# Performance work log

Hardware: AMD Instinct MI355X
Metric: run time of the kernel (lower is better)

The kernel has to match this reference:

```python
import jax, jax.numpy as jnp
import numpy as np

HIDDEN = 640
NQ = 10      # query heads
NKV = 2      # kv heads
HD = HIDDEN // NQ   # 64
GROUPS = NQ // NKV  # 5
THETA = 500000.0
EPS = 1e-6


def rmsnorm(x, g):
    rms = jnp.sqrt(jnp.mean(x * x, axis=-1, keepdims=True) + EPS)
    return x / rms * g


def bitlinear(x, w, g):
    """RMSNorm + ternary weight / int8 activation fake-quant + GEMM + rescale."""
    x = rmsnorm(x, g)
    alpha = jnp.maximum(jnp.mean(jnp.abs(w)), 1e-10)
    w_q = jnp.clip(jnp.round(w / alpha), -1.0, 1.0)
    w_q = w + jax.lax.stop_gradient(w_q - w)            # STE
    gamma = jnp.maximum(jnp.max(jnp.abs(x), axis=-1, keepdims=True), 1e-10)
    x_q = jnp.clip(jnp.round(x * 127.0 / gamma), -128.0, 127.0)
    x_q = x + jax.lax.stop_gradient(x_q - x)            # STE
    return (x_q @ w_q.T) * (alpha * gamma / 127.0)


def rope_tables(L):
    # half-dim cos/sin tables [L, HD//2]; equivalent to the torch code's
    # repeat_interleave followed by [..., ::2] slicing.
    freqs = 1.0 / THETA ** (jnp.arange(0, HD, 2, dtype=jnp.float32) / HD)
    ang = jnp.arange(L, dtype=jnp.float32)[:, None] * freqs[None, :]
    return jnp.cos(ang), jnp.sin(ang)


def apply_rope(x, cos, sin):
    # x: [B,H,L,D]; cos/sin: [L,D/2] broadcast over B,H
    x1 = x[..., ::2]
    x2 = x[..., 1::2]
    o1 = x1 * cos - x2 * sin
    o2 = x2 * cos + x1 * sin
    return jnp.stack([o1, o2], axis=-1).reshape(x.shape)


def setup_inputs() -> dict:
    key = jax.random.key(0)
    ks = jax.random.split(key, 6)
    B, L = 32, 512
    x = jax.random.normal(ks[0], (B, L, HIDDEN), dtype=jnp.float32)
    s_h = 1.0 / np.sqrt(HIDDEN)
    q_w = jax.random.normal(ks[1], (NQ * HD, HIDDEN), dtype=jnp.float32) * s_h
    k_w = jax.random.normal(ks[2], (NKV * HD, HIDDEN), dtype=jnp.float32) * s_h
    v_w = jax.random.normal(ks[3], (NKV * HD, HIDDEN), dtype=jnp.float32) * s_h
    o_w = jax.random.normal(ks[4], (HIDDEN, NQ * HD), dtype=jnp.float32) * (1.0 / np.sqrt(NQ * HD))
    ones = jnp.ones((HIDDEN,), dtype=jnp.float32)
    return {
        "x": x,
        "norm_w": ones,
        "q_w": q_w, "q_g": ones,
        "k_w": k_w, "k_g": ones,
        "v_w": v_w, "v_g": ones,
        "o_w": o_w, "o_g": jnp.ones((NQ * HD,), dtype=jnp.float32),
    }


def reference(x, norm_w, q_w, q_g, k_w, k_g, v_w, v_g, o_w, o_g):
    B, L, _ = x.shape
    residual = x
    h = rmsnorm(x, norm_w)
    q = bitlinear(h, q_w, q_g).reshape(B, L, NQ, HD).transpose(0, 2, 1, 3)
    k = bitlinear(h, k_w, k_g).reshape(B, L, NKV, HD).transpose(0, 2, 1, 3)
    v = bitlinear(h, v_w, v_g).reshape(B, L, NKV, HD).transpose(0, 2, 1, 3)
    cos, sin = rope_tables(L)
    q = apply_rope(q, cos, sin)
    k = apply_rope(k, cos, sin)
    k = jnp.repeat(k, GROUPS, axis=1)   # [B,NQ,L,HD]
    v = jnp.repeat(v, GROUPS, axis=1)
    scale = 1.0 / np.sqrt(HD).astype(np.float32)
    attn = jnp.einsum("bhqd,bhkd->bhqk", q, k) * scale
    attn = jax.nn.softmax(attn, axis=-1)
    out = jnp.einsum("bhqk,bhkd->bhqd", attn, v)
    out = out.transpose(0, 2, 1, 3).reshape(B, L, NQ * HD)
    return bitlinear(out, o_w, o_g) + residual
```

## Files before the change

### kernel.cpp

```cpp
#include <hip/hip_runtime.h>
#include <math.h>
#include <stdint.h>

#define HIDDEN 640
#define NTOK   16384
#define LSEQ   512
#define BATCH  32
#define NQH    10
#define NKVH   2
#define HDIM   64
#define GROUPS 5

typedef int      int4v  __attribute__((ext_vector_type(4)));
typedef int      int16v __attribute__((ext_vector_type(16)));
typedef _Float16 f16x8  __attribute__((ext_vector_type(8)));
typedef _Float16 f16x2  __attribute__((ext_vector_type(2)));
typedef float    f32x4  __attribute__((ext_vector_type(4)));

__device__ __forceinline__ float wred_sum(float v){
  #pragma unroll
  for (int m=1;m<64;m<<=1) v += __shfl_xor(v,m);
  return v;
}
__device__ __forceinline__ float wred_max(float v){
  #pragma unroll
  for (int m=1;m<64;m<<=1) v = fmaxf(v,__shfl_xor(v,m));
  return v;
}
__device__ __forceinline__ f16x2 pkmax(f16x2 a, f16x2 b){
  f16x2 r;
  r.x = (a.x > b.x) ? a.x : b.x;
  r.y = (a.y > b.y) ? a.y : b.y;
  return r;
}
__device__ __forceinline__ f16x2 shflx(f16x2 v, int m){
  int t = __builtin_bit_cast(int, v);
  t = __shfl_xor(t, m);
  return __builtin_bit_cast(f16x2, t);
}

__global__ __launch_bounds__(256) void absum4_kernel(
    const float* __restrict__ w0, const float* __restrict__ w1,
    const float* __restrict__ w2, const float* __restrict__ w3,
    float* __restrict__ sums){
  const float* w; int n;
  switch(blockIdx.y){
    case 0:  w=w0; n=640*640; break;
    case 1:  w=w1; n=128*640; break;
    case 2:  w=w2; n=128*640; break;
    default: w=w3; n=640*640; break;
  }
  __shared__ float red[256];
  int tid = threadIdx.x;
  float s = 0.f;
  for (int i = blockIdx.x*256 + tid; i < n; i += gridDim.x*256) s += fabsf(w[i]);
  red[tid] = s; __syncthreads();
  for (int off=128; off>0; off>>=1){ if (tid<off) red[tid]+=red[tid+off]; __syncthreads(); }
  if (tid==0) atomicAdd(&sums[blockIdx.y], red[0]);
}

__global__ __launch_bounds__(256) void wquant4_kernel(
    const float* __restrict__ w0, const float* __restrict__ w1,
    const float* __restrict__ w2, const float* __restrict__ w3,
    int8_t* __restrict__ o0, int8_t* __restrict__ o1,
    int8_t* __restrict__ o2, int8_t* __restrict__ o3,
    const float* __restrict__ sums){
  const float* w; int8_t* o; int n;
  switch(blockIdx.y){
    case 0:  w=w0; o=o0; n=640*640; break;
    case 1:  w=w1; o=o1; n=128*640; break;
    case 2:  w=w2; o=o2; n=128*640; break;
    default: w=w3; o=o3; n=640*640; break;
  }
  float alpha = fmaxf(sums[blockIdx.y]/(float)n, 1e-10f);
  float inva  = 1.0f/alpha;
  int i = blockIdx.x*256 + threadIdx.x;
  if (i < n){
    float t = rintf(w[i]*inva);
    t = fminf(1.f, fmaxf(-1.f, t));
    int nr = i/640;
    int kc = i - nr*640;
    int flat = (((nr>>5)*20 + (kc>>5))<<10) + (((((kc>>4)&1)<<5) | (nr&31))<<4) + (kc&15);
    o[flat] = (int8_t)t;
  }
}

__global__ __launch_bounds__(256) void token_prep_kernel(
    const float* __restrict__ x, const float* __restrict__ nw,
    const float* __restrict__ qg, const float* __restrict__ kg, const float* __restrict__ vg,
    int8_t* __restrict__ xqq, int8_t* __restrict__ xqk, int8_t* __restrict__ xqv,
    float* __restrict__ gq, float* __restrict__ gk, float* __restrict__ gv){
  int lane = threadIdx.x & 63;
  int m = blockIdx.x*4 + (threadIdx.x>>6);
  const float* xr = x + (size_t)m*HIDDEN;
  float xv[10], h[10];
  float ss = 0.f;
  #pragma unroll
  for (int j=0;j<10;j++){ float t = xr[lane + 64*j]; xv[j]=t; ss += t*t; }
  float inv1 = 1.0f/sqrtf(wred_sum(ss)*(1.0f/HIDDEN) + 1e-6f);
  float ss2 = 0.f;
  #pragma unroll
  for (int j=0;j<10;j++){ float t = xv[j]*inv1*nw[lane+64*j]; h[j]=t; ss2 += t*t; }
  float inv2 = 1.0f/sqrtf(wred_sum(ss2)*(1.0f/HIDDEN) + 1e-6f);

  const float* gs[3] = {qg, kg, vg};
  int8_t* outs[3] = {xqq, xqk, xqv};
  float* gams[3] = {gq, gk, gv};
  #pragma unroll
  for (int s=0;s<3;s++){
    const float* g = gs[s];
    float t[10], amax = 0.f;
    #pragma unroll
    for (int j=0;j<10;j++){ float v = h[j]*inv2*g[lane+64*j]; t[j]=v; amax = fmaxf(amax, fabsf(v)); }
    float gamma = fmaxf(wred_max(amax), 1e-10f);
    float sc = 127.0f/gamma;
    int8_t* dst = outs[s] + (size_t)m*HIDDEN;
    #pragma unroll
    for (int j=0;j<10;j++){
      float v = rintf(t[j]*sc);
      v = fminf(127.f, fmaxf(-128.f, v));
      dst[lane+64*j] = (int8_t)v;
    }
    if (lane==0) gams[s][m] = gamma;
  }
}

__global__ __launch_bounds__(256) void o_prep_kernel(const _Float16* __restrict__ ao,
    const float* __restrict__ og, int8_t* __restrict__ xqo, float* __restrict__ go){
  int lane = threadIdx.x & 63;
  int m = blockIdx.x*4 + (threadIdx.x>>6);
  const _Float16* xr = ao + (size_t)m*HIDDEN;
  float xv[10];
  float ss = 0.f;
  #pragma unroll
  for (int j=0;j<10;j++){ float t = (float)xr[lane + 64*j]; xv[j]=t; ss += t*t; }
  float inv = 1.0f/sqrtf(wred_sum(ss)*(1.0f/HIDDEN) + 1e-6f);
  float t[10], amax = 0.f;
  #pragma unroll
  for (int j=0;j<10;j++){ float v = xv[j]*inv*og[lane+64*j]; t[j]=v; amax = fmaxf(amax, fabsf(v)); }
  float gamma = fmaxf(wred_max(amax), 1e-10f);
  float sc = 127.0f/gamma;
  int8_t* dst = xqo + (size_t)m*HIDDEN;
  #pragma unroll
  for (int j=0;j<10;j++){
    float v = rintf(t[j]*sc);
    v = fminf(127.f, fmaxf(-128.f, v));
    dst[lane+64*j] = (int8_t)v;
  }
  if (lane==0) go[m] = gamma;
}

__device__ __forceinline__ void gemm_core(
    const int8_t* __restrict__ xq, const int8_t* __restrict__ wqf,
    int m0, int n0, int lane, int16v& acc0, int16v& acc1){
  int half = lane >> 5, lan5 = lane & 31;
  const int8_t* arow = xq + (size_t)(m0 + lan5)*HIDDEN + half*16;
  const int8_t* b0 = wqf + (((size_t)(n0>>5)    *20)<<10) + (lane<<4);
  const int8_t* b1 = wqf + (((size_t)((n0>>5)+1)*20)<<10) + (lane<<4);
  #pragma unroll
  for (int kb=0; kb<20; kb++){
    int4v a  = *(const int4v*)(arow + kb*32);
    int4v v0 = *(const int4v*)(b0 + (kb<<10));
    int4v v1 = *(const int4v*)(b1 + (kb<<10));
    acc0 = __builtin_amdgcn_mfma_i32_32x32x32_i8(a, v0, acc0, 0, 0, 0);
    acc1 = __builtin_amdgcn_mfma_i32_32x32x32_i8(a, v1, acc1, 0, 0, 0);
  }
}

__global__ __launch_bounds__(256) void qkv_gemm_kernel(
    const int8_t* __restrict__ xq_q, const float* __restrict__ g_q, const int8_t* __restrict__ wq_q,
    const int8_t* __restrict__ xq_k, const float* __restrict__ g_k, const int8_t* __restrict__ wq_k,
    const int8_t* __restrict__ xq_v, const float* __restrict__ g_v, const int8_t* __restrict__ wq_v,
    const float* __restrict__ sums,
    _Float16* __restrict__ qbuf, _Float16* __restrict__ kbuf, _Float16* __restrict__ vbuf){
  __shared__ _Float16 Tr[4][64][40];
  int bx = blockIdx.x;
  const int8_t *xq, *wq; const float* gam; _Float16* outh;
  int n0, aidx, nheads, mode; float inv_nw, vscale;
  if (bx < 10){ xq=xq_q; wq=wq_q; gam=g_q; outh=qbuf; n0=bx*64;      aidx=0; inv_nw=1.0f/409600.f; nheads=NQH;  mode=1; vscale=0.125f; }
  else if (bx < 12){ xq=xq_k; wq=wq_k; gam=g_k; outh=kbuf; n0=(bx-10)*64; aidx=1; inv_nw=1.0f/81920.f; nheads=NKVH; mode=1; vscale=1.0f; }
  else { xq=xq_v; wq=wq_v; gam=g_v; outh=vbuf; n0=(bx-12)*64; aidx=2; inv_nw=1.0f/81920.f; nheads=NKVH; mode=2; vscale=1.0f; }

  int lane = threadIdx.x & 63;
  int w    = threadIdx.x >> 6;
  int m0   = blockIdx.y*128 + w*32;
  int half = lane >> 5, lan5 = lane & 31;

  int16v acc0 = {0}, acc1 = {0};
  gemm_core(xq, wq, m0, n0, lane, acc0, acc1);

  float alpha = fmaxf(sums[aidx]*inv_nw, 1e-10f);
  float fr0 = 0.f, fr1 = 0.f;
  if (mode == 1){
    int d0 = (lan5) & ~1;
    int d1 = (32 + lan5) & ~1;
    fr0 = __expf(-(float)d0*(1.0f/64.0f)*13.122363377404328f);
    fr1 = __expf(-(float)d1*(1.0f/64.0f)*13.122363377404328f);
  }

  #pragma unroll
  for (int reg=0; reg<16; reg++){
    int ml = (reg&3) + 8*(reg>>2) + 4*half;
    int m = m0 + ml;
    float sc = alpha*gam[m]*(1.0f/127.0f);
    float v0 = (float)acc0[reg]*sc;
    float v1 = (float)acc1[reg]*sc;
    if (mode == 1){
      int b = m >> 9, l = m & 511;
      int head = n0 >> 6;
      float p0 = __shfl_xor(v0, 1);
      float p1 = __shfl_xor(v1, 1);
      float sn0, cs0, sn1, cs1;
      __sincosf((float)l*fr0, &sn0, &cs0);
      __sincosf((float)l*fr1, &sn1, &cs1);
      if (lane & 1){ v0 = v0*cs0 + p0*sn0;  v1 = v1*cs1 + p1*sn1; }
      else         { v0 = v0*cs0 - p0*sn0;  v1 = v1*cs1 - p1*sn1; }
      _Float16* dst = outh + ((((size_t)b*nheads + head)*LSEQ + l)<<6);
      dst[lan5]      = (_Float16)(v0*vscale);
      dst[32 + lan5] = (_Float16)(v1*vscale);
    } else {
      Tr[w][lan5][ml]      = (_Float16)v0;
      Tr[w][32 + lan5][ml] = (_Float16)v1;
    }
  }
  if (mode == 2){
    int b = m0 >> 9, l0 = m0 & 511;
    int head = n0 >> 6;
    f16x8 r0 = *(const f16x8*)&Tr[w][lane][0];
    f16x8 r1 = *(const f16x8*)&Tr[w][lane][8];
    f16x8 r2 = *(const f16x8*)&Tr[w][lane][16];
    f16x8 r3 = *(const f16x8*)&Tr[w][lane][24];
    _Float16* dst = outh + (((size_t)b*nheads + head)*HDIM + lane)*LSEQ + l0;
    ((f16x8*)dst)[0] = r0;
    ((f16x8*)dst)[1] = r1;
    ((f16x8*)dst)[2] = r2;
    ((f16x8*)dst)[3] = r3;
  }
}

__global__ __launch_bounds__(256) void out_gemm_kernel(
    const int8_t* __restrict__ xq, const float* __restrict__ gam,
    const int8_t* __restrict__ wq, const float* __restrict__ sums,
    const float* __restrict__ resid, float* __restrict__ outf){
  int lane = threadIdx.x & 63;
  int w    = threadIdx.x >> 6;
  int m0   = blockIdx.y*128 + w*32;
  int n0   = blockIdx.x*64;
  int half = lane >> 5, lan5 = lane & 31;

  int16v acc0 = {0}, acc1 = {0};
  gemm_core(xq, wq, m0, n0, lane, acc0, acc1);

  float alpha = fmaxf(sums[3]*(1.0f/409600.f), 1e-10f);
  #pragma unroll
  for (int reg=0; reg<16; reg++){
    int m = m0 + (reg&3) + 8*(reg>>2) + 4*half;
    float sc = alpha*gam[m]*(1.0f/127.0f);
    size_t ofs = (size_t)m*HIDDEN;
    outf[ofs + n0 + lan5]      = (float)acc0[reg]*sc + resid[ofs + n0 + lan5];
    outf[ofs + n0 + 32 + lan5] = (float)acc1[reg]*sc + resid[ofs + n0 + 32 + lan5];
  }
}

__device__ __forceinline__ int kv_addr(int row, int chunk){
  return (row<<6) + (((chunk ^ (row&7)))<<3);
}

__device__ __forceinline__ void softmax_update(
    f32x4* S, float* m_i, float* l_i, f32x4* O,
    _Float16 (*PsRow)[72], int quad, int c){
  float mxr[4], psr[4];
  #pragma unroll
  for (int r=0;r<4;r++)
    mxr[r] = fmaxf(fmaxf(S[0][r],S[1][r]), fmaxf(S[2][r],S[3][r]));
  f16x2 a01 = {(_Float16)mxr[0], (_Float16)mxr[1]};
  f16x2 a23 = {(_Float16)mxr[2], (_Float16)mxr[3]};
  #pragma unroll
  for (int mm=1; mm<16; mm<<=1){
    a01 = pkmax(a01, shflx(a01, mm));
    a23 = pkmax(a23, shflx(a23, mm));
  }
  float mn[4] = {(float)a01.x, (float)a01.y, (float)a23.x, (float)a23.y};
  #pragma unroll
  for (int r=0;r<4;r++){
    float mnew = fmaxf(m_i[r], mn[r]);
    float af = __expf(m_i[r] - mnew);
    m_i[r] = mnew;
    float ps = 0.f;
    #pragma unroll
    for (int nt=0;nt<4;nt++){
      float p = __expf(S[nt][r] - mnew);
      ps += p;
      PsRow[(quad<<2)+r][(nt<<4)+c] = (_Float16)p;
    }
    psr[r] = ps;
    l_i[r] *= af;
    O[0][r]*=af; O[1][r]*=af; O[2][r]*=af; O[3][r]*=af;
  }
  f16x2 s01 = {(_Float16)psr[0], (_Float16)psr[1]};
  f16x2 s23 = {(_Float16)psr[2], (_Float16)psr[3]};
  #pragma unroll
  for (int mm=1; mm<16; mm<<=1){
    s01 = s01 + shflx(s01, mm);
    s23 = s23 + shflx(s23, mm);
  }
  l_i[0] += (float)s01.x; l_i[1] += (float)s01.y;
  l_i[2] += (float)s23.x; l_i[3] += (float)s23.y;
}

__global__ __launch_bounds__(256,2) void attn_mfma_kernel(
    const _Float16* __restrict__ q, const _Float16* __restrict__ k,
    const _Float16* __restrict__ vt, _Float16* __restrict__ o){
  __shared__ _Float16 Ks[2][64*64];
  __shared__ _Float16 Vs[2][64*64];
  __shared__ _Float16 Ps[4][32][72];
  int tid  = threadIdx.x;
  int wv   = tid >> 6, lane = tid & 63;
  int quad = lane >> 4, c = lane & 15;
  int h = blockIdx.y, b = blockIdx.z;
  int hk = h / GROUPS;
  int qrow0 = blockIdx.x*128 + wv*32;

  const _Float16* qb = q + ((size_t)((b*NQH+h)*LSEQ) + qrow0 + c)*HDIM + quad*8;
  f16x8 qa0 = *(const f16x8*)qb;
  f16x8 qa1 = *(const f16x8*)(qb + 32);
  f16x8 qb0 = *(const f16x8*)(qb + 16*HDIM);
  f16x8 qb1 = *(const f16x8*)(qb + 16*HDIM + 32);

  const _Float16* kbase = k  + (size_t)((b*NKVH+hk)*LSEQ)*HDIM;
  const _Float16* vbase = vt + (size_t)((b*NKVH+hk)*HDIM)*LSEQ;

  int srow = tid >> 3, schunk = tid & 7;
  const _Float16* kg0 = kbase + (size_t)srow*HDIM      + schunk*8;
  const _Float16* kg1 = kbase + (size_t)(srow+32)*HDIM + schunk*8;
  const _Float16* vg0 = vbase + (size_t)srow*LSEQ      + schunk*8;
  const _Float16* vg1 = vbase + (size_t)(srow+32)*LSEQ + schunk*8;
  int ka0 = kv_addr(srow,    schunk);
  int ka1 = kv_addr(srow+32, schunk);

  {
    f16x8 t0 = *(const f16x8*)kg0;
    f16x8 t1 = *(const f16x8*)kg1;
    f16x8 t2 = *(const f16x8*)vg0;
    f16x8 t3 = *(const f16x8*)vg1;
    *(f16x8*)&Ks[0][ka0] = t0;
    *(f16x8*)&Ks[0][ka1] = t1;
    *(f16x8*)&Vs[0][ka0] = t2;
    *(f16x8*)&Vs[0][ka1] = t3;
  }

  f32x4 O0[4] = {{0,0,0,0},{0,0,0,0},{0,0,0,0},{0,0,0,0}};
  f32x4 O1[4] = {{0,0,0,0},{0,0,0,0},{0,0,0,0},{0,0,0,0}};
  float m0_[4] = {-INFINITY,-INFINITY,-INFINITY,-INFINITY};
  float m1_[4] = {-INFINITY,-INFINITY,-INFINITY,-INFINITY};
  float l0_[4] = {0,0,0,0}, l1_[4] = {0,0,0,0};
  f16x8 pk0, pk1, pv0, pv1;

  for (int kt=0; kt<8; kt++){
    __syncthreads();
    int cur = kt & 1, nxt = cur ^ 1;
    if (kt < 7){
      pk0 = *(const f16x8*)(kg0 + (size_t)(kt+1)*64*HDIM);
      pk1 = *(const f16x8*)(kg1 + (size_t)(kt+1)*64*HDIM);
      pv0 = *(const f16x8*)(vg0 + (kt+1)*64);
      pv1 = *(const f16x8*)(vg1 + (kt+1)*64);
    }
    f32x4 S0[4], S1[4];
    #pragma unroll
    for (int nt=0; nt<4; nt++){
      int row = (nt<<4) + c;
      f16x8 kf0 = *(const f16x8*)&Ks[cur][kv_addr(row, quad)];
      f16x8 kf1 = *(const f16x8*)&Ks[cur][kv_addr(row, quad+4)];
      f32x4 s = {0,0,0,0};
      s = __builtin_amdgcn_mfma_f32_16x16x32_f16(qa0, kf0, s, 0,0,0);
      s = __builtin_amdgcn_mfma_f32_16x16x32_f16(qa1, kf1, s, 0,0,0);
      S0[nt] = s;
      f32x4 s2 = {0,0,0,0};
      s2 = __builtin_amdgcn_mfma_f32_16x16x32_f16(qb0, kf0, s2, 0,0,0);
      s2 = __builtin_amdgcn_mfma_f32_16x16x32_f16(qb1, kf1, s2, 0,0,0);
      S1[nt] = s2;
    }
    softmax_update(S0, m0_, l0_, O0, (_Float16(*)[72])&Ps[wv][0],  quad, c);
    softmax_update(S1, m1_, l1_, O1, (_Float16(*)[72])&Ps[wv][16], quad, c);
    f16x8 p00 = *(const f16x8*)&Ps[wv][c][quad*8];
    f16x8 p01 = *(const f16x8*)&Ps[wv][c][quad*8 + 32];
    f16x8 p10 = *(const f16x8*)&Ps[wv][16+c][quad*8];
    f16x8 p11 = *(const f16x8*)&Ps[wv][16+c][quad*8 + 32];
    #pragma unroll
    for (int nt=0;nt<4;nt++){
      int row = (nt<<4) + c;
      f16x8 vf0 = *(const f16x8*)&Vs[cur][kv_addr(row, quad)];
      f16x8 vf1 = *(const f16x8*)&Vs[cur][kv_addr(row, quad+4)];
      O0[nt] = __builtin_amdgcn_mfma_f32_16x16x32_f16(p00, vf0, O0[nt], 0,0,0);
      O0[nt] = __builtin_amdgcn_mfma_f32_16x16x32_f16(p01, vf1, O0[nt], 0,0,0);
      O1[nt] = __builtin_amdgcn_mfma_f32_16x16x32_f16(p10, vf0, O1[nt], 0,0,0);
      O1[nt] = __builtin_amdgcn_mfma_f32_16x16x32_f16(p11, vf1, O1[nt], 0,0,0);
    }
    if (kt < 7){
      *(f16x8*)&Ks[nxt][ka0] = pk0;
      *(f16x8*)&Ks[nxt][ka1] = pk1;
      *(f16x8*)&Vs[nxt][ka0] = pv0;
      *(f16x8*)&Vs[nxt][ka1] = pv1;
    }
  }
  #pragma unroll
  for (int r=0;r<4;r++){
    float invl0 = 1.0f/l0_[r];
    float invl1 = 1.0f/l1_[r];
    int m0 = (b<<9) + qrow0 + (quad<<2) + r;
    _Float16* d0 = o + (size_t)m0*HIDDEN + (h<<6);
    _Float16* d1 = o + (size_t)(m0+16)*HIDDEN + (h<<6);
    #pragma unroll
    for (int nt=0;nt<4;nt++){
      d0[(nt<<4)+c] = (_Float16)(O0[nt][r]*invl0);
      d1[(nt<<4)+c] = (_Float16)(O1[nt][r]*invl1);
    }
  }
}

extern "C" void kernel_launch(void* const* d_in, const int* in_sizes, int n_in,
                              void* d_out, int out_size, void* d_ws, size_t ws_size,
                              hipStream_t stream){
  (void)in_sizes; (void)n_in; (void)out_size; (void)ws_size;
  const float* x  = (const float*)d_in[0];
  const float* nw = (const float*)d_in[1];
  const float* qw = (const float*)d_in[2];
  const float* qg = (const float*)d_in[3];
  const float* kw = (const float*)d_in[4];
  const float* kg = (const float*)d_in[5];
  const float* vw = (const float*)d_in[6];
  const float* vg = (const float*)d_in[7];
  const float* ow = (const float*)d_in[8];
  const float* og = (const float*)d_in[9];
  float* out = (float*)d_out;

  char* base = (char*)d_ws;
  size_t off = 0;
  auto alloc = [&](size_t nbytes)->void*{
    off = (off + 255) & ~(size_t)255;
    void* p = base + off;
    off += nbytes;
    return p;
  };
  float*  sums = (float*) alloc(4*sizeof(float));
  int8_t* wq_q = (int8_t*)alloc(640*640);
  int8_t* wq_k = (int8_t*)alloc(128*640);
  int8_t* wq_v = (int8_t*)alloc(128*640);
  int8_t* wq_o = (int8_t*)alloc(640*640);
  int8_t* xq_q = (int8_t*)alloc((size_t)NTOK*HIDDEN);
  int8_t* xq_k = (int8_t*)alloc((size_t)NTOK*HIDDEN);
  int8_t* xq_v = (int8_t*)alloc((size_t)NTOK*HIDDEN);
  int8_t* xq_o = (int8_t*)alloc((size_t)NTOK*HIDDEN);
  float*  g_q  = (float*) alloc((size_t)NTOK*4);
  float*  g_k  = (float*) alloc((size_t)NTOK*4);
  float*  g_v  = (float*) alloc((size_t)NTOK*4);
  float*  g_o  = (float*) alloc((size_t)NTOK*4);
  _Float16* qbuf = (_Float16*)alloc((size_t)BATCH*NQH *LSEQ*HDIM*2);
  _Float16* kbuf = (_Float16*)alloc((size_t)BATCH*NKVH*LSEQ*HDIM*2);
  _Float16* vbuf = (_Float16*)alloc((size_t)BATCH*NKVH*LSEQ*HDIM*2);
  _Float16* abuf = (_Float16*)alloc((size_t)NTOK*HIDDEN*2);

  (void)hipMemsetAsync(sums, 0, 4*sizeof(float), stream);
  absum4_kernel<<<dim3(64,4),256,0,stream>>>(qw, kw, vw, ow, sums);
  wquant4_kernel<<<dim3(1600,4),256,0,stream>>>(qw, kw, vw, ow, wq_q, wq_k, wq_v, wq_o, sums);

  token_prep_kernel<<<NTOK/4,256,0,stream>>>(x, nw, qg, kg, vg, xq_q, xq_k, xq_v, g_q, g_k, g_v);

  qkv_gemm_kernel<<<dim3(14,128),256,0,stream>>>(xq_q, g_q, wq_q,
                                                 xq_k, g_k, wq_k,
                                                 xq_v, g_v, wq_v,
                                                 sums, qbuf, kbuf, vbuf);

  attn_mfma_kernel<<<dim3(4,NQH,BATCH),256,0,stream>>>(qbuf, kbuf, vbuf, abuf);

  o_prep_kernel<<<NTOK/4,256,0,stream>>>(abuf, og, xq_o, g_o);
  out_gemm_kernel<<<dim3(10,128),256,0,stream>>>(xq_o, g_o, wq_o, sums, x, out);
}
```

Measured before the change: 266.3 us.

## Write quantized activations in MFMA fragment layout and use exp2 softmax

The token and o-projection prep kernels now write int8 activations directly in the same 32x32 MFMA fragment-tiled layout used for the weights. The GEMM core can then load A fragments with contiguous 16-byte per-lane loads instead of strided row reads. Separately, the Q scale folds log2(e) into 1/sqrt(d) so the softmax can use exp2f instead of __expf. The cost is scattered byte stores in the prep kernels.

```diff
diff --git a/kernel.cpp b/kernel.cpp
--- a/kernel.cpp
+++ b/kernel.cpp
@@ -37,6 +37,10 @@
   int t = __builtin_bit_cast(int, v);
   t = __shfl_xor(t, m);
   return __builtin_bit_cast(f16x2, t);
+}
+
+__device__ __forceinline__ int frag_flat(int m, int k){
+  return (((m>>5)*20 + (k>>5))<<10) + (((((k>>4)&1)<<5) | (m&31))<<4) + (k&15);
 }
 
 __global__ __launch_bounds__(256) void absum4_kernel(
@@ -80,8 +84,7 @@
     t = fminf(1.f, fmaxf(-1.f, t));
     int nr = i/640;
     int kc = i - nr*640;
-    int flat = (((nr>>5)*20 + (kc>>5))<<10) + (((((kc>>4)&1)<<5) | (nr&31))<<4) + (kc&15);
-    o[flat] = (int8_t)t;
+    o[frag_flat(nr, kc)] = (int8_t)t;
   }
 }
 
@@ -93,6 +96,8 @@
   int lane = threadIdx.x & 63;
   int m = blockIdx.x*4 + (threadIdx.x>>6);
   const float* xr = x + (size_t)m*HIDDEN;
+  int abase = ((m>>5)*20480) + ((m&31)<<4)
+            + ((lane>>5)<<10) + (((lane>>4)&1)<<9) + (lane&15);
   float xv[10], h[10];
   float ss = 0.f;
   #pragma unroll
@@ -114,12 +119,12 @@
     for (int j=0;j<10;j++){ float v = h[j]*inv2*g[lane+64*j]; t[j]=v; amax = fmaxf(amax, fabsf(v)); }
     float gamma = fmaxf(wred_max(amax), 1e-10f);
     float sc = 127.0f/gamma;
-    int8_t* dst = outs[s] + (size_t)m*HIDDEN;
+    int8_t* dst = outs[s] + abase;
     #pragma unroll
     for (int j=0;j<10;j++){
       float v = rintf(t[j]*sc);
       v = fminf(127.f, fmaxf(-128.f, v));
-      dst[lane+64*j] = (int8_t)v;
+      dst[j*2048] = (int8_t)v;
     }
     if (lane==0) gams[s][m] = gamma;
   }
@@ -130,6 +135,8 @@
   int lane = threadIdx.x & 63;
   int m = blockIdx.x*4 + (threadIdx.x>>6);
   const _Float16* xr = ao + (size_t)m*HIDDEN;
+  int abase = ((m>>5)*20480) + ((m&31)<<4)
+            + ((lane>>5)<<10) + (((lane>>4)&1)<<9) + (lane&15);
   float xv[10];
   float ss = 0.f;
   #pragma unroll
@@ -140,12 +147,12 @@
   for (int j=0;j<10;j++){ float v = xv[j]*inv*og[lane+64*j]; t[j]=v; amax = fmaxf(amax, fabsf(v)); }
   float gamma = fmaxf(wred_max(amax), 1e-10f);
   float sc = 127.0f/gamma;
-  int8_t* dst = xqo + (size_t)m*HIDDEN;
+  int8_t* dst = xqo + abase;
   #pragma unroll
   for (int j=0;j<10;j++){
     float v = rintf(t[j]*sc);
     v = fminf(127.f, fmaxf(-128.f, v));
-    dst[lane+64*j] = (int8_t)v;
+    dst[j*2048] = (int8_t)v;
   }
   if (lane==0) go[m] = gamma;
 }
@@ -153,13 +160,12 @@
 __device__ __forceinline__ void gemm_core(
     const int8_t* __restrict__ xq, const int8_t* __restrict__ wqf,
     int m0, int n0, int lane, int16v& acc0, int16v& acc1){
-  int half = lane >> 5, lan5 = lane & 31;
-  const int8_t* arow = xq + (size_t)(m0 + lan5)*HIDDEN + half*16;
-  const int8_t* b0 = wqf + (((size_t)(n0>>5)    *20)<<10) + (lane<<4);
-  const int8_t* b1 = wqf + (((size_t)((n0>>5)+1)*20)<<10) + (lane<<4);
+  const int8_t* a0 = xq  + (size_t)(m0>>5)*20480 + (lane<<4);
+  const int8_t* b0 = wqf + (size_t)(n0>>5)*20480 + (lane<<4);
+  const int8_t* b1 = b0 + 20480;
   #pragma unroll
   for (int kb=0; kb<20; kb++){
-    int4v a  = *(const int4v*)(arow + kb*32);
+    int4v a  = *(const int4v*)(a0 + (kb<<10));
     int4v v0 = *(const int4v*)(b0 + (kb<<10));
     int4v v1 = *(const int4v*)(b1 + (kb<<10));
     acc0 = __builtin_amdgcn_mfma_i32_32x32x32_i8(a, v0, acc0, 0, 0, 0);
@@ -177,7 +183,7 @@
   int bx = blockIdx.x;
   const int8_t *xq, *wq; const float* gam; _Float16* outh;
   int n0, aidx, nheads, mode; float inv_nw, vscale;
-  if (bx < 10){ xq=xq_q; wq=wq_q; gam=g_q; outh=qbuf; n0=bx*64;      aidx=0; inv_nw=1.0f/409600.f; nheads=NQH;  mode=1; vscale=0.125f; }
+  if (bx < 10){ xq=xq_q; wq=wq_q; gam=g_q; outh=qbuf; n0=bx*64;      aidx=0; inv_nw=1.0f/409600.f; nheads=NQH;  mode=1; vscale=0.18033688011110918f; }
   else if (bx < 12){ xq=xq_k; wq=wq_k; gam=g_k; outh=kbuf; n0=(bx-10)*64; aidx=1; inv_nw=1.0f/81920.f; nheads=NKVH; mode=1; vscale=1.0f; }
   else { xq=xq_v; wq=wq_v; gam=g_v; outh=vbuf; n0=(bx-12)*64; aidx=2; inv_nw=1.0f/81920.f; nheads=NKVH; mode=2; vscale=1.0f; }
 
@@ -284,12 +290,12 @@
   #pragma unroll
   for (int r=0;r<4;r++){
     float mnew = fmaxf(m_i[r], mn[r]);
-    float af = __expf(m_i[r] - mnew);
+    float af = exp2f(m_i[r] - mnew);
     m_i[r] = mnew;
     float ps = 0.f;
     #pragma unroll
     for (int nt=0;nt<4;nt++){
-      float p = __expf(S[nt][r] - mnew);
+      float p = exp2f(S[nt][r] - mnew);
       ps += p;
       PsRow[(quad<<2)+r][(nt<<4)+c] = (_Float16)p;
     }
```

Result: faster. 259.0 us (-2.7%).
